# Optimization experiments

Measured on AMD Instinct MI355X. Metric: run time of the kernel, lower is better.

The kernel has to match this reference:

```python
import jax, jax.numpy as jnp
import numpy as np

S, B, E, H = 2048, 4, 1024, 16
D = E // H


def setup_inputs() -> dict:
    key = jax.random.key(0)
    ks = jax.random.split(key, 12)
    scale = 1.0 / np.sqrt(E)
    inp = {
        "query": jax.random.normal(ks[0], (S, B, E), jnp.float32),
        "key": jax.random.normal(ks[1], (S, B, E), jnp.float32),
        "value": jax.random.normal(ks[2], (S, B, E), jnp.float32),
        # causal mask: True = masked out (matches masked_fill semantics)
        "attn_mask": jnp.triu(jnp.ones((S, S), jnp.bool_), k=1),
        "Wq": jax.random.normal(ks[3], (E, E), jnp.float32) * scale,
        "bq": jax.random.normal(ks[4], (E,), jnp.float32) * scale,
        "Wk": jax.random.normal(ks[5], (E, E), jnp.float32) * scale,
        "bk": jax.random.normal(ks[6], (E,), jnp.float32) * scale,
        "Wv": jax.random.normal(ks[7], (E, E), jnp.float32) * scale,
        "bv": jax.random.normal(ks[8], (E,), jnp.float32) * scale,
        "Wo": jax.random.normal(ks[9], (E, E), jnp.float32) * scale,
        "bo": jax.random.normal(ks[10], (E,), jnp.float32) * scale,
    }
    return inp


def reference(query, key, value, attn_mask, Wq, bq, Wk, bk, Wv, bv, Wo, bo):
    # inputs are [S, B, E]; torch Linear: y = x @ W.T + b
    def proj_heads(x, W, b):
        y = jnp.einsum("sbe,fe->sbf", x, W) + b          # [S,B,E]
        return y.transpose(1, 0, 2).reshape(B, S, H, D).transpose(0, 2, 1, 3)  # [B,H,S,D]

    Q = proj_heads(query, Wq, bq)
    K = proj_heads(key, Wk, bk)
    V = proj_heads(value, Wv, bv)

    scores = jnp.einsum("bhsd,bhtd->bhst", Q, K) / jnp.sqrt(jnp.float32(D))
    scores = jnp.where(attn_mask[None, None, :, :], -jnp.inf, scores)
    probs = jax.nn.softmax(scores, axis=-1)              # dropout p=0 -> identity

    ctx = jnp.einsum("bhst,bhtd->bhsd", probs, V)        # [B,H,S,D]
    ctx = ctx.transpose(0, 2, 1, 3).reshape(B, S, E).transpose(1, 0, 2)  # [S,B,E]

    out = jnp.einsum("sbe,fe->sbf", ctx, Wo) + bo        # [S,B,E]
    attn_map = probs.mean(axis=1)                        # [B,S,S]
    return out, attn_map
```

## Files before the change

### kernel.cpp

```cpp
#include <hip/hip_runtime.h>
#include <stdint.h>

#define S_LEN 2048
#define B_SZ  4
#define E_SZ  1024
#define H_CNT 16
#define D_HD  64

typedef __attribute__((ext_vector_type(4))) float          f32x4;
typedef __attribute__((ext_vector_type(2))) float          f32x2;
typedef __attribute__((ext_vector_type(8))) __bf16         bf16x8;
typedef __attribute__((ext_vector_type(4))) unsigned short u16x4;
typedef __attribute__((ext_vector_type(4))) int            i32x4;
typedef __attribute__((ext_vector_type(2))) int            i32x2;
typedef unsigned short us;

#define QSCALE 0.1803368801111204f

__device__ __forceinline__ us bfu(float f) {
    __bf16 h = (__bf16)f;
    return __builtin_bit_cast(us, h);
}
__device__ __forceinline__ unsigned pk2(float a, float b) {
    return (unsigned)bfu(a) | ((unsigned)bfu(b) << 16);
}
#define EXP2(x) __builtin_amdgcn_exp2f(x)
#define MFMA(a, b, c) __builtin_amdgcn_mfma_f32_16x16x32_bf16((a), (b), (c), 0, 0, 0)

__device__ __forceinline__ void gll16(const void* g, void* l) {
    __builtin_amdgcn_global_load_lds(
        (const __attribute__((address_space(1))) void*)g,
        (__attribute__((address_space(3))) void*)l, 16, 0, 0);
}

__global__ __launch_bounds__(256)
void convert_many(const float* __restrict__ s0, const float* __restrict__ s1,
                  const float* __restrict__ s2, const float* __restrict__ s3,
                  us* __restrict__ d0, us* __restrict__ d1,
                  us* __restrict__ d2, us* __restrict__ d3,
                  float sc0)
{
    const int which = blockIdx.y;
    const float* s = which == 0 ? s0 : which == 1 ? s1 : which == 2 ? s2 : s3;
    us* d = which == 0 ? d0 : which == 1 ? d1 : which == 2 ? d2 : d3;
    const float sc = which == 0 ? sc0 : 1.0f;
    const int i = blockIdx.x * 256 + threadIdx.x;
    f32x4 v = ((const f32x4*)s)[i];
    u16x4 o;
    o.x = bfu(v.x * sc); o.y = bfu(v.y * sc);
    o.z = bfu(v.z * sc); o.w = bfu(v.w * sc);
    ((u16x4*)d)[i] = o;
}

template<bool AF32, bool OUT_QKV>
__global__ __launch_bounds__(256)
void gemm_bt(const void* __restrict__ Ap,
             const us* __restrict__ Bw,
             const float* __restrict__ bias, float bscale,
             void* __restrict__ Outp)
{
    __shared__ us Al[2][128 * 64];
    __shared__ us Bl[2][128 * 64];

    const int t     = threadIdx.x;
    const int lane  = t & 63;
    const int wave  = t >> 6;
    const int lrow  = lane & 15;
    const int lk    = lane >> 4;
    const int bm    = (blockIdx.x >> 3) << 7;
    const int bn    = (blockIdx.x & 7) << 7;
    const int wr    = (wave >> 1) << 6;
    const int wc    = (wave & 1) << 6;
    const int srow8 = lane >> 3;
    const int scol  = (lane & 7) << 3;

    f32x4 acc[4][4];
    #pragma unroll
    for (int i = 0; i < 4; ++i)
        #pragma unroll
        for (int j = 0; j < 4; ++j) acc[i][j] = (f32x4)0.0f;

    #define GSTAGE(k0_, dst_)                                                        \
        _Pragma("unroll")                                                            \
        for (int j_ = 0; j_ < 4; ++j_) {                                             \
            const int chunk_ = wave * 4 + j_;                                        \
            const int r_ = chunk_ * 8 + srow8;                                       \
            gll16((const us*)Ap + (size_t)(bm + r_) * E_SZ + (k0_) + scol,           \
                  &Al[dst_][chunk_ * 512]);                                          \
            gll16(Bw + (size_t)(bn + r_) * E_SZ + (k0_) + scol,                      \
                  &Bl[dst_][chunk_ * 512]);                                          \
        }

    #define GCOMP(src_)                                                              \
        _Pragma("unroll")                                                            \
        for (int kk = 0; kk < 2; ++kk) {                                             \
            bf16x8 af[4], bfr[4];                                                    \
            _Pragma("unroll")                                                        \
            for (int i = 0; i < 4; ++i)                                              \
                af[i] = *(const bf16x8*)(&Al[src_][(wr + i*16 + lrow) * 64 + kk*32 + lk*8]); \
            _Pragma("unroll")                                                        \
            for (int j = 0; j < 4; ++j)                                              \
                bfr[j] = *(const bf16x8*)(&Bl[src_][(wc + j*16 + lrow) * 64 + kk*32 + lk*8]); \
            _Pragma("unroll")                                                        \
            for (int i = 0; i < 4; ++i)                                              \
                _Pragma("unroll")                                                    \
                for (int j = 0; j < 4; ++j)                                          \
                    acc[i][j] = MFMA(af[i], bfr[j], acc[i][j]);                      \
        }

    if (AF32) {
        for (int k0 = 0; k0 < E_SZ; k0 += 64) {
            __syncthreads();
            #pragma unroll
            for (int j = 0; j < 4; ++j) {
                const int chunk = wave * 4 + j;
                const int r = chunk * 8 + srow8;
                const float* ga = (const float*)Ap + (size_t)(bm + r) * E_SZ + k0 + scol;
                f32x4 u0 = *(const f32x4*)ga;
                f32x4 u1 = *(const f32x4*)(ga + 4);
                i32x4 wv;
                wv.x = (int)pk2(u0.x, u0.y); wv.y = (int)pk2(u0.z, u0.w);
                wv.z = (int)pk2(u1.x, u1.y); wv.w = (int)pk2(u1.z, u1.w);
                *(i32x4*)(&Al[0][chunk * 512 + lane * 8]) = wv;
                gll16(Bw + (size_t)(bn + r) * E_SZ + k0 + scol, &Bl[0][chunk * 512]);
            }
            __syncthreads();
            GCOMP(0);
        }
    } else {
        GSTAGE(0, 0);
        __syncthreads();
        int buf = 0;
        #pragma unroll 2
        for (int kt = 0; kt < 15; ++kt) {
            GSTAGE((kt + 1) * 64, buf ^ 1);
            GCOMP(buf);
            __syncthreads();
            buf ^= 1;
        }
        GCOMP(buf);
    }
    #undef GSTAGE
    #undef GCOMP

    const int crow = lk << 2;
    #pragma unroll
    for (int i = 0; i < 4; ++i) {
        #pragma unroll
        for (int j = 0; j < 4; ++j) {
            const int n = bn + wc + j*16 + lrow;
            const float bv = bias[n] * bscale;
            #pragma unroll
            for (int r = 0; r < 4; ++r) {
                const int m = bm + wr + i*16 + crow + r;
                const float val = acc[i][j][r] + bv;
                if (OUT_QKV) {
                    const int s = m >> 2, b = m & 3;
                    const int h = n >> 6, d = n & 63;
                    ((us*)Outp)[((size_t)(b*H_CNT + h)*S_LEN + s)*D_HD + d] = bfu(val);
                } else {
                    ((float*)Outp)[(size_t)m * E_SZ + n] = val;
                }
            }
        }
    }
}

__global__ __launch_bounds__(512, 6)
void flash_fwd(const us* __restrict__ Qb,
               const us* __restrict__ Kb,
               const us* __restrict__ Vb,
               us* __restrict__ ctx,
               float* __restrict__ mout,
               float* __restrict__ lout)
{
    __shared__ us Kl[2][64 * 64];
    __shared__ us Vt[2][64 * 72];
    __shared__ us Pl[8][16 * 72];

    const int t    = threadIdx.x;
    const int lane = t & 63, wave = t >> 6;
    const int lrow = lane & 15, lk = lane >> 4;
    const int bh   = blockIdx.x & 63;
    const int qt   = 15 - (blockIdx.x >> 6);
    const int b    = bh >> 4, h = bh & 15;

    const size_t base = (size_t)bh * S_LEN * D_HD;
    const us* Q = Qb + base;
    const us* K = Kb + base;
    const us* V = Vb + base;

    const int qbase = qt * 128 + wave * 16;
    const int myq   = qbase + lrow;
    us* pl = &Pl[wave][0];

    bf16x8 qf[2];
    #pragma unroll
    for (int ks = 0; ks < 2; ++ks)
        qf[ks] = *(const bf16x8*)(Q + (size_t)myq * D_HD + ks*32 + lk*8);

    f32x4 ctxa[4];
    #pragma unroll
    for (int nf = 0; nf < 4; ++nf) ctxa[nf] = (f32x4)0.0f;
    float mst = -__builtin_inff(), lst = 0.0f;

    const int tU  = t & 255;
    const int vp2 = (tU & 31) << 1;
    const int vd8 = (tU >> 5) << 3;

    i32x4 v0, v1;

    #define STAGE_K(kv_, kl_)                                                        \
        if (t < 256) {                                                               \
            _Pragma("unroll")                                                        \
            for (int i_ = 0; i_ < 2; ++i_) {                                         \
                const int row_  = i_*32 + (t >> 3);                                  \
                const int slot_ = (t & 7) ^ (row_ & 7);                              \
                gll16(K + (size_t)((kv_) + row_)*D_HD + slot_*8,                     \
                      (kl_) + i_*2048 + ((t >> 6) << 9));                            \
            }                                                                        \
        }
    #define LOAD_V(kv_)                                                             \
        if (t >= 256) {                                                              \
            const us* vp_ = V + (size_t)((kv_) + vp2)*D_HD + vd8;                    \
            v0 = *(const i32x4*)vp_;                                                 \
            v1 = *(const i32x4*)(vp_ + D_HD);                                        \
        }
    #define WRITE_V(vt_)                                                             \
        if (t >= 256) {                                                              \
            union { i32x4 v; us s[8]; } ua_, ub_; ua_.v = v0; ub_.v = v1;            \
            _Pragma("unroll")                                                        \
            for (int j_ = 0; j_ < 8; ++j_) {                                         \
                unsigned w_ = (unsigned)ua_.s[j_] | ((unsigned)ub_.s[j_] << 16);     \
                *(unsigned*)((vt_) + (vd8 + j_)*72 + vp2) = w_;                      \
            }                                                                        \
        }

    STAGE_K(0, Kl[0]);
    LOAD_V(0);
    WRITE_V(Vt[0]);
    __syncthreads();

    const int kvend = qt*128 + 128;
    int cur = 0;
    for (int kv = 0; kv < kvend; kv += 64) {
        const bool more = (kv + 64) < kvend;
        if (more) {
            STAGE_K(kv + 64, Kl[cur ^ 1]);
            LOAD_V(kv + 64);
        }

        if (kv <= qbase) {
            const us* kl = Kl[cur];
            const us* vt = Vt[cur];
            f32x4 sa[4];
            #pragma unroll
            for (int nf = 0; nf < 4; ++nf) sa[nf] = (f32x4)0.0f;
            #pragma unroll
            for (int ks = 0; ks < 2; ++ks)
                #pragma unroll
                for (int nf = 0; nf < 4; ++nf) {
                    const int key = nf*16 + lrow;
                    bf16x8 kf = *(const bf16x8*)((const char*)kl + (key << 7) +
                                    (((((ks << 2) | lk)) ^ (lrow & 7)) << 4));
                    sa[nf] = MFMA(kf, qf[ks], sa[nf]);
                }
            if (kv + 63 > qbase) {
                #pragma unroll
                for (int nf = 0; nf < 4; ++nf)
                    #pragma unroll
                    for (int r = 0; r < 4; ++r)
                        if (kv + nf*16 + (lk << 2) + r > myq) sa[nf][r] = -__builtin_inff();
            }
            float pmax = sa[0][0];
            #pragma unroll
            for (int nf = 0; nf < 4; ++nf)
                #pragma unroll
                for (int r = 0; r < 4; ++r) pmax = fmaxf(pmax, sa[nf][r]);
            pmax = fmaxf(pmax, __shfl_xor(pmax, 16));
            pmax = fmaxf(pmax, __shfl_xor(pmax, 32));
            const bool skip = __all(pmax <= mst + 8.0f);
            if (!skip) {
                const float mnew  = fmaxf(mst, pmax);
                const float alpha = EXP2(mst - mnew);
                mst = mnew;
                lst *= alpha;
                float ar[4];
                #pragma unroll
                for (int r = 0; r < 4; ++r) ar[r] = __shfl(alpha, (lk << 2) + r);
                #pragma unroll
                for (int nf = 0; nf < 4; ++nf)
                    #pragma unroll
                    for (int r = 0; r < 4; ++r) ctxa[nf][r] *= ar[r];
            }
            float sum = 0.0f;
            #pragma unroll
            for (int nf = 0; nf < 4; ++nf)
                #pragma unroll
                for (int r = 0; r < 4; ++r) {
                    const float p = EXP2(sa[nf][r] - mst);
                    sa[nf][r] = p;
                    sum += p;
                }
            sum += __shfl_xor(sum, 16);
            sum += __shfl_xor(sum, 32);
            lst += sum;
            #pragma unroll
            for (int nf = 0; nf < 4; ++nf) {
                i32x2 dw;
                dw.x = (int)pk2(sa[nf][0], sa[nf][1]);
                dw.y = (int)pk2(sa[nf][2], sa[nf][3]);
                *(i32x2*)(pl + lrow*72 + nf*16 + (lk << 2)) = dw;
            }
            #pragma unroll
            for (int ks = 0; ks < 2; ++ks) {
                bf16x8 pa = *(const bf16x8*)(pl + lrow*72 + ks*32 + lk*8);
                #pragma unroll
                for (int nf = 0; nf < 4; ++nf) {
                    bf16x8 vf = *(const bf16x8*)(vt + (nf*16 + lrow)*72 + ks*32 + lk*8);
                    ctxa[nf] = MFMA(pa, vf, ctxa[nf]);
                }
            }
        }

        if (more) { WRITE_V(Vt[cur ^ 1]); }
        __syncthreads();
        cur ^= 1;
    }

    const float inv = 1.0f / lst;
    float invr[4];
    #pragma unroll
    for (int r = 0; r < 4; ++r) invr[r] = __shfl(inv, (lk << 2) + r);
    #pragma unroll
    for (int nf = 0; nf < 4; ++nf)
        #pragma unroll
        for (int r = 0; r < 4; ++r) {
            const int srow = qbase + (lk << 2) + r;
            const int d    = nf*16 + lrow;
            ctx[((size_t)srow * B_SZ + b) * E_SZ + h*D_HD + d] = bfu(ctxa[nf][r] * invr[r]);
        }
    if (lane < 16) {
        mout[(size_t)bh * S_LEN + myq] = mst;
        lout[(size_t)bh * S_LEN + myq] = inv * 0.0625f;
    }
    #undef STAGE_K
    #undef LOAD_V
    #undef WRITE_V
}

__global__ __launch_bounds__(512, 4)
void attn_map_k(const us* __restrict__ Qb,
                const us* __restrict__ Kb,
                const float* __restrict__ mrows,
                const float* __restrict__ lrows,
                float* __restrict__ map)
{
    const int t  = threadIdx.x;
    const int jt = blockIdx.x & 15;
    const int it = (blockIdx.x >> 4) & 15;
    const int b  = blockIdx.x >> 8;
    float* mt = map + ((size_t)b * S_LEN + it*128) * S_LEN + jt*128;

    if (jt > it) {
        f32x4 z = (f32x4)0.0f;
        #pragma unroll
        for (int i = 0; i < 8; ++i) {
            const int c = i*512 + t;
            *(f32x4*)(mt + (size_t)(c >> 5) * S_LEN + (c & 31) * 4) = z;
        }
        return;
    }

    __shared__ us Ql[128 * 64];
    __shared__ us Kl[128 * 64];
    __shared__ f32x2 Mll[16 * 128];

    const int lane = t & 63, wave = t >> 6;
    const int lrow = lane & 15, lk = lane >> 4;
    const int wr = (wave >> 1) << 5;
    const int wc = (wave & 1) << 6;

    #pragma unroll
    for (int i = 0; i < 4; ++i) {
        const int idx = i*512 + t;
        const int h = idx >> 7, row = idx & 127;
        f32x2 v;
        v.x = mrows[(size_t)(b*H_CNT + h)*S_LEN + it*128 + row];
        v.y = lrows[(size_t)(b*H_CNT + h)*S_LEN + it*128 + row];
        Mll[idx] = v;
    }

    f32x4 pacc[2][4];
    #pragma unroll
    for (int i = 0; i < 2; ++i)
        #pragma unroll
        for (int j = 0; j < 4; ++j) pacc[i][j] = (f32x4)0.0f;

    const int qrow  = it*128;
    const int krow  = jt*128;
    const int srow  = t >> 3;
    const int sslot = t & 7;

    for (int h = 0; h < H_CNT; ++h) {
        const size_t base = (size_t)(b*H_CNT + h) * S_LEN * D_HD;
        const us* Qh = Qb + base + (size_t)qrow * D_HD;
        const us* Kh = Kb + base + (size_t)krow * D_HD;
        __syncthreads();
        #pragma unroll
        for (int i = 0; i < 2; ++i) {
            const int row  = i*64 + srow;
            const int slot = sslot ^ (row & 7);
            gll16(Qh + (size_t)row * D_HD + slot*8, &Ql[i*4096 + ((t >> 6) << 9)]);
            gll16(Kh + (size_t)row * D_HD + slot*8, &Kl[i*4096 + ((t >> 6) << 9)]);
        }
        __syncthreads();

        bf16x8 kf[4][2];
        #pragma unroll
        for (int nf = 0; nf < 4; ++nf)
            #pragma unroll
            for (int ks = 0; ks < 2; ++ks) {
                const int row = wc + nf*16 + lrow;
                kf[nf][ks] = *(const bf16x8*)(&Kl[row*64 + (((ks<<2)|lk) ^ (row&7))*8]);
            }

        #pragma unroll
        for (int mf = 0; mf < 2; ++mf) {
            const int arow = wr + mf*16 + lrow;
            bf16x8 af0 = *(const bf16x8*)(&Ql[arow*64 + ((lk)     ^ (arow&7))*8]);
            bf16x8 af1 = *(const bf16x8*)(&Ql[arow*64 + ((4 | lk) ^ (arow&7))*8]);
            f32x2 ml[4];
            #pragma unroll
            for (int r = 0; r < 4; ++r)
                ml[r] = Mll[h*128 + wr + mf*16 + (lk << 2) + r];
            #pragma unroll
            for (int nf = 0; nf < 4; ++nf) {
                f32x4 sa = (f32x4)0.0f;
                sa = MFMA(af0, kf[nf][0], sa);
                sa = MFMA(af1, kf[nf][1], sa);
                #pragma unroll
                for (int r = 0; r < 4; ++r)
                    pacc[mf][nf][r] += EXP2(sa[r] - ml[r].x) * ml[r].y;
            }
        }
    }

    #pragma unroll
    for (int mf = 0; mf < 2; ++mf)
        #pragma unroll
        for (int nf = 0; nf < 4; ++nf)
            #pragma unroll
            for (int r = 0; r < 4; ++r) {
                const int row = wr + mf*16 + (lk << 2) + r;
                const int col = wc + nf*16 + lrow;
                float v = pacc[mf][nf][r];
                if (it == jt && col > row) v = 0.0f;
                mt[(size_t)row * S_LEN + col] = v;
            }
}

extern "C" void kernel_launch(void* const* d_in, const int* in_sizes, int n_in,
                              void* d_out, int out_size, void* d_ws, size_t ws_size,
                              hipStream_t stream)
{
    const float* q_in = (const float*)d_in[0];
    const float* k_in = (const float*)d_in[1];
    const float* v_in = (const float*)d_in[2];
    const float* Wq = (const float*)d_in[4];
    const float* bq = (const float*)d_in[5];
    const float* Wk = (const float*)d_in[6];
    const float* bk = (const float*)d_in[7];
    const float* Wv = (const float*)d_in[8];
    const float* bv = (const float*)d_in[9];
    const float* Wo = (const float*)d_in[10];
    const float* bo = (const float*)d_in[11];

    const size_t EE   = (size_t)E_SZ * E_SZ;
    const size_t BHSD = (size_t)B_SZ * H_CNT * S_LEN * D_HD;
    const size_t SBE  = (size_t)S_LEN * B_SZ * E_SZ;

    us* Wqb = (us*)d_ws;
    us* Wkb = Wqb + EE;
    us* Wvb = Wkb + EE;
    us* Wob = Wvb + EE;
    us* base = Wob + EE;

    const size_t need_big = (4*EE + 6*BHSD) * sizeof(us);
    const bool big = ws_size >= need_big;

    us *Aq, *Ak, *Av, *Qb, *Kb, *Vb, *ctx;
    float* ml;
    if (big) {
        Aq = base;       Ak = Aq + BHSD;  Av = Ak + BHSD;
        Qb = Av + BHSD;  Kb = Qb + BHSD;  Vb = Kb + BHSD;
        ctx = Aq;
        ml  = (float*)Ak;
    } else {
        Aq = Ak = Av = nullptr;
        Qb = base;       Kb = Qb + BHSD;  Vb = Kb + BHSD;
        ctx = Vb + BHSD;
        ml  = (float*)(ctx + SBE);
    }
    float* mrows = ml;
    float* lrows = ml + (size_t)B_SZ * H_CNT * S_LEN;

    float* out = (float*)d_out;
    float* map = out + SBE;

    convert_many<<<dim3(1024, 4), 256, 0, stream>>>(Wq, Wk, Wv, Wo, Wqb, Wkb, Wvb, Wob, QSCALE);

    if (big) {
        convert_many<<<dim3(8192, 3), 256, 0, stream>>>(q_in, k_in, v_in, nullptr,
                                                        Aq, Ak, Av, nullptr, 1.0f);
        gemm_bt<false, true><<<512, 256, 0, stream>>>(Aq, Wqb, bq, QSCALE, Qb);
        gemm_bt<false, true><<<512, 256, 0, stream>>>(Ak, Wkb, bk, 1.0f,   Kb);
        gemm_bt<false, true><<<512, 256, 0, stream>>>(Av, Wvb, bv, 1.0f,   Vb);
    } else {
        gemm_bt<true, true><<<512, 256, 0, stream>>>(q_in, Wqb, bq, QSCALE, Qb);
        gemm_bt<true, true><<<512, 256, 0, stream>>>(k_in, Wkb, bk, 1.0f,   Kb);
        gemm_bt<true, true><<<512, 256, 0, stream>>>(v_in, Wvb, bv, 1.0f,   Vb);
    }

    flash_fwd<<<1024, 512, 0, stream>>>(Qb, Kb, Vb, ctx, mrows, lrows);

    gemm_bt<false, false><<<512, 256, 0, stream>>>(ctx, Wob, bo, 1.0f, d_out);

    attn_map_k<<<B_SZ*16*16, 512, 0, stream>>>(Qb, Kb, mrows, lrows, map);
}
```

Measured before the change: 256.6 us.

## Process two 16-row query groups per wave in flash attention, halving block size

Each wave of flash_fwd now handles 32 query rows as two 16-row groups, reusing every K fragment and V fragment loaded from LDS across both groups. The block shrinks from 512 to 256 threads, and all threads now share the K and V staging work. This is meant to cut LDS read traffic per MFMA and improve register-level reuse. In exchange it roughly doubles the accumulator and softmax state held per wave, which raises register pressure and may lower occupancy. It also coarsens the causal-mask granularity per wave.

Result: slower. 262.9 us (+2.5%).

```diff
diff --git a/kernel.cpp b/kernel.cpp
--- a/kernel.cpp
+++ b/kernel.cpp
@@ -166,7 +166,7 @@
     }
 }
 
-__global__ __launch_bounds__(512, 6)
+__global__ __launch_bounds__(256, 3)
 void flash_fwd(const us* __restrict__ Qb,
                const us* __restrict__ Kb,
                const us* __restrict__ Vb,
@@ -176,7 +176,7 @@
 {
     __shared__ us Kl[2][64 * 64];
     __shared__ us Vt[2][64 * 72];
-    __shared__ us Pl[8][16 * 72];
+    __shared__ us Pl[4][16 * 72];
 
     const int t    = threadIdx.x;
     const int lane = t & 63, wave = t >> 6;
@@ -190,28 +190,32 @@
     const us* K = Kb + base;
     const us* V = Vb + base;
 
-    const int qbase = qt * 128 + wave * 16;
-    const int myq   = qbase + lrow;
+    const int qbase = qt * 128 + wave * 32;
     us* pl = &Pl[wave][0];
 
-    bf16x8 qf[2];
-    #pragma unroll
-    for (int ks = 0; ks < 2; ++ks)
-        qf[ks] = *(const bf16x8*)(Q + (size_t)myq * D_HD + ks*32 + lk*8);
-
-    f32x4 ctxa[4];
-    #pragma unroll
-    for (int nf = 0; nf < 4; ++nf) ctxa[nf] = (f32x4)0.0f;
-    float mst = -__builtin_inff(), lst = 0.0f;
-
-    const int tU  = t & 255;
-    const int vp2 = (tU & 31) << 1;
-    const int vd8 = (tU >> 5) << 3;
+    bf16x8 qf[2][2];
+    #pragma unroll
+    for (int g = 0; g < 2; ++g)
+        #pragma unroll
+        for (int ks = 0; ks < 2; ++ks)
+            qf[g][ks] = *(const bf16x8*)(Q + (size_t)(qbase + g*16 + lrow)*D_HD + ks*32 + lk*8);
+
+    f32x4 ctxa[2][4];
+    float mst[2], lst[2];
+    #pragma unroll
+    for (int g = 0; g < 2; ++g) {
+        #pragma unroll
+        for (int nf = 0; nf < 4; ++nf) ctxa[g][nf] = (f32x4)0.0f;
+        mst[g] = -__builtin_inff(); lst[g] = 0.0f;
+    }
+
+    const int vp2 = (t & 31) << 1;
+    const int vd8 = (t >> 5) << 3;
 
     i32x4 v0, v1;
 
     #define STAGE_K(kv_, kl_)                                                        \
-        if (t < 256) {                                                               \
+        {                                                                            \
             _Pragma("unroll")                                                        \
             for (int i_ = 0; i_ < 2; ++i_) {                                         \
                 const int row_  = i_*32 + (t >> 3);                                  \
@@ -221,13 +225,13 @@
             }                                                                        \
         }
     #define LOAD_V(kv_)                                                             \
-        if (t >= 256) {                                                              \
+        {                                                                            \
             const us* vp_ = V + (size_t)((kv_) + vp2)*D_HD + vd8;                    \
             v0 = *(const i32x4*)vp_;                                                 \
             v1 = *(const i32x4*)(vp_ + D_HD);                                        \
         }
     #define WRITE_V(vt_)                                                             \
-        if (t >= 256) {                                                              \
+        {                                                                            \
             union { i32x4 v; us s[8]; } ua_, ub_; ua_.v = v0; ub_.v = v1;            \
             _Pragma("unroll")                                                        \
             for (int j_ = 0; j_ < 8; ++j_) {                                         \
@@ -250,12 +254,14 @@
             LOAD_V(kv + 64);
         }
 
-        if (kv <= qbase) {
+        if (kv <= qbase + 16) {
             const us* kl = Kl[cur];
             const us* vt = Vt[cur];
-            f32x4 sa[4];
-            #pragma unroll
-            for (int nf = 0; nf < 4; ++nf) sa[nf] = (f32x4)0.0f;
+            f32x4 sa[2][4];
+            #pragma unroll
+            for (int g = 0; g < 2; ++g)
+                #pragma unroll
+                for (int nf = 0; nf < 4; ++nf) sa[g][nf] = (f32x4)0.0f;
             #pragma unroll
             for (int ks = 0; ks < 2; ++ks)
                 #pragma unroll
@@ -263,62 +269,79 @@
                     const int key = nf*16 + lrow;
                     bf16x8 kf = *(const bf16x8*)((const char*)kl + (key << 7) +
                                     (((((ks << 2) | lk)) ^ (lrow & 7)) << 4));
-                    sa[nf] = MFMA(kf, qf[ks], sa[nf]);
+                    sa[0][nf] = MFMA(kf, qf[0][ks], sa[0][nf]);
+                    sa[1][nf] = MFMA(kf, qf[1][ks], sa[1][nf]);
                 }
-            if (kv + 63 > qbase) {
+            #pragma unroll
+            for (int g = 0; g < 2; ++g) {
+                const int qb_g = qbase + g*16;
+                if (kv <= qb_g) {
+                    const int myq = qb_g + lrow;
+                    if (kv + 63 > qb_g) {
+                        #pragma unroll
+                        for (int nf = 0; nf < 4; ++nf)
+                            #pragma unroll
+                            for (int r = 0; r < 4; ++r)
+                                if (kv + nf*16 + (lk << 2) + r > myq) sa[g][nf][r] = -__builtin_inff();
+                    }
+                    float pmax = sa[g][0][0];
+                    #pragma unroll
+                    for (int nf = 0; nf < 4; ++nf)
+                        #pragma unroll
+                        for (int r = 0; r < 4; ++r) pmax = fmaxf(pmax, sa[g][nf][r]);
+                    pmax = fmaxf(pmax, __shfl_xor(pmax, 16));
+                    pmax = fmaxf(pmax, __shfl_xor(pmax, 32));
+                    const bool skip = __all(pmax <= mst[g] + 8.0f);
+                    if (!skip) {
+                        const float mnew  = fmaxf(mst[g], pmax);
+                        const float alpha = EXP2(mst[g] - mnew);
+                        mst[g] = mnew;
+                        lst[g] *= alpha;
+                        float ar[4];
+                        #pragma unroll
+                        for (int r = 0; r < 4; ++r) ar[r] = __shfl(alpha, (lk << 2) + r);
+                        #pragma unroll
+                        for (int nf = 0; nf < 4; ++nf)
+                            #pragma unroll
+                            for (int r = 0; r < 4; ++r) ctxa[g][nf][r] *= ar[r];
+                    }
+                    float sum = 0.0f;
+                    #pragma unroll
+                    for (int nf = 0; nf < 4; ++nf)
+                        #pragma unroll
+                        for (int r = 0; r < 4; ++r) {
+                            const float p = EXP2(sa[g][nf][r] - mst[g]);
+                            sa[g][nf][r] = p;
+                            sum += p;
+                        }
+                    sum += __shfl_xor(sum, 16);
+                    sum += __shfl_xor(sum, 32);
+                    lst[g] += sum;
+                }
+            }
+            bf16x8 vf[2][4];
+            #pragma unroll
+            for (int ks = 0; ks < 2; ++ks)
                 #pragma unroll
                 for (int nf = 0; nf < 4; ++nf)
+                    vf[ks][nf] = *(const bf16x8*)(vt + (nf*16 + lrow)*72 + ks*32 + lk*8);
+            #pragma unroll
+            for (int g = 0; g < 2; ++g) {
+                if (kv <= qbase + g*16) {
                     #pragma unroll
-                    for (int r = 0; r < 4; ++r)
-                        if (kv + nf*16 + (lk << 2) + r > myq) sa[nf][r] = -__builtin_inff();
-            }
-            float pmax = sa[0][0];
-            #pragma unroll
-            for (int nf = 0; nf < 4; ++nf)
-                #pragma unroll
-                for (int r = 0; r < 4; ++r) pmax = fmaxf(pmax, sa[nf][r]);
-            pmax = fmaxf(pmax, __shfl_xor(pmax, 16));
-            pmax = fmaxf(pmax, __shfl_xor(pmax, 32));
-            const bool skip = __all(pmax <= mst + 8.0f);
-            if (!skip) {
-                const float mnew  = fmaxf(mst, pmax);
-                const float alpha = EXP2(mst - mnew);
-                mst = mnew;
-                lst *= alpha;
-                float ar[4];
-                #pragma unroll
-                for (int r = 0; r < 4; ++r) ar[r] = __shfl(alpha, (lk << 2) + r);
-                #pragma unroll
-                for (int nf = 0; nf < 4; ++nf)
+                    for (int nf = 0; nf < 4; ++nf) {
+                        i32x2 dw;
+                        dw.x = (int)pk2(sa[g][nf][0], sa[g][nf][1]);
+                        dw.y = (int)pk2(sa[g][nf][2], sa[g][nf][3]);
+                        *(i32x2*)(pl + lrow*72 + nf*16 + (lk << 2)) = dw;
+                    }
                     #pragma unroll
-                    for (int r = 0; r < 4; ++r) ctxa[nf][r] *= ar[r];
-            }
-            float sum = 0.0f;
-            #pragma unroll
-            for (int nf = 0; nf < 4; ++nf)
-                #pragma unroll
-                for (int r = 0; r < 4; ++r) {
-                    const float p = EXP2(sa[nf][r] - mst);
-                    sa[nf][r] = p;
-                    sum += p;
-                }
-            sum += __shfl_xor(sum, 16);
-            sum += __shfl_xor(sum, 32);
-            lst += sum;
-            #pragma unroll
-            for (int nf = 0; nf < 4; ++nf) {
-                i32x2 dw;
-                dw.x = (int)pk2(sa[nf][0], sa[nf][1]);
-                dw.y = (int)pk2(sa[nf][2], sa[nf][3]);
-                *(i32x2*)(pl + lrow*72 + nf*16 + (lk << 2)) = dw;
-            }
-            #pragma unroll
-            for (int ks = 0; ks < 2; ++ks) {
-                bf16x8 pa = *(const bf16x8*)(pl + lrow*72 + ks*32 + lk*8);
-                #pragma unroll
-                for (int nf = 0; nf < 4; ++nf) {
-                    bf16x8 vf = *(const bf16x8*)(vt + (nf*16 + lrow)*72 + ks*32 + lk*8);
-                    ctxa[nf] = MFMA(pa, vf, ctxa[nf]);
+                    for (int ks = 0; ks < 2; ++ks) {
+                        bf16x8 pa = *(const bf16x8*)(pl + lrow*72 + ks*32 + lk*8);
+                        #pragma unroll
+                        for (int nf = 0; nf < 4; ++nf)
+                            ctxa[g][nf] = MFMA(pa, vf[ks][nf], ctxa[g][nf]);
+                    }
                 }
             }
         }
@@ -328,21 +351,25 @@
         cur ^= 1;
     }
 
-    const float inv = 1.0f / lst;
-    float invr[4];
-    #pragma unroll
-    for (int r = 0; r < 4; ++r) invr[r] = __shfl(inv, (lk << 2) + r);
-    #pragma unroll
-    for (int nf = 0; nf < 4; ++nf)
-        #pragma unroll
-        for (int r = 0; r < 4; ++r) {
-            const int srow = qbase + (lk << 2) + r;
-            const int d    = nf*16 + lrow;
-            ctx[((size_t)srow * B_SZ + b) * E_SZ + h*D_HD + d] = bfu(ctxa[nf][r] * invr[r]);
-        }
-    if (lane < 16) {
-        mout[(size_t)bh * S_LEN + myq] = mst;
-        lout[(size_t)bh * S_LEN + myq] = inv * 0.0625f;
+    #pragma unroll
+    for (int g = 0; g < 2; ++g) {
+        const float inv = 1.0f / lst[g];
+        float invr[4];
+        #pragma unroll
+        for (int r = 0; r < 4; ++r) invr[r] = __shfl(inv, (lk << 2) + r);
+        #pragma unroll
+        for (int nf = 0; nf < 4; ++nf)
+            #pragma unroll
+            for (int r = 0; r < 4; ++r) {
+                const int srow = qbase + g*16 + (lk << 2) + r;
+                const int d    = nf*16 + lrow;
+                ctx[((size_t)srow * B_SZ + b) * E_SZ + h*D_HD + d] = bfu(ctxa[g][nf][r] * invr[r]);
+            }
+        if (lane < 16) {
+            const int myq = qbase + g*16 + lrow;
+            mout[(size_t)bh * S_LEN + myq] = mst[g];
+            lout[(size_t)bh * S_LEN + myq] = inv * 0.0625f;
+        }
     }
     #undef STAGE_K
     #undef LOAD_V
@@ -522,7 +549,7 @@
         gemm_bt<true, true><<<512, 256, 0, stream>>>(v_in, Wvb, bv, 1.0f,   Vb);
     }
 
-    flash_fwd<<<1024, 512, 0, stream>>>(Qb, Kb, Vb, ctx, mrows, lrows);
+    flash_fwd<<<1024, 256, 0, stream>>>(Qb, Kb, Vb, ctx, mrows, lrows);
 
     gemm_bt<false, false><<<512, 256, 0, stream>>>(ctx, Wob, bo, 1.0f, d_out);
 
```
